# Kernel optimization log

Hardware: AMD Instinct MI355X
Metric: run time of the kernel (lower is better)

## Reference

```python
import jax, jax.numpy as jnp
from jax import lax
import numpy as np

NUM_TOKENS = 2048
HIDDEN = 768
MAX_SPAN_WIDTH = 20
NUM_CAND = NUM_TOKENS * MAX_SPAN_WIDTH  # 40960
FEAT = 20
UNARY = 1024
SPAN_DIM = 3 * HIDDEN + FEAT  # 2324
MAX_NUM_SPANS = 512
TOP_SPAN_RATIO = 0.4


def setup_inputs() -> dict:
    key = jax.random.key(0)
    ks = jax.random.split(key, 16)
    starts = jax.random.randint(ks[0], (NUM_CAND,), 0, NUM_TOKENS, dtype=jnp.int32)
    widths = jax.random.randint(ks[1], (NUM_CAND,), 0, MAX_SPAN_WIDTH, dtype=jnp.int32)
    ends = jnp.minimum(starts + widths, NUM_TOKENS - 1)
    p = lambda k, shp: (0.02 * jax.random.normal(k, shp, dtype=jnp.float32))
    return {
        "hidden_states": jax.random.normal(ks[2], (NUM_TOKENS, HIDDEN), dtype=jnp.float32),
        "candidate_starts": starts,
        "candidate_ends": ends,
        "speaker_ids": jax.random.randint(ks[3], (NUM_TOKENS,), 0, 2, dtype=jnp.int32),
        "w_attn": p(ks[4], (HIDDEN,)),
        "b_attn": p(ks[5], ()),
        "W1": p(ks[6], (SPAN_DIM, UNARY)),
        "b1": p(ks[7], (UNARY,)),
        "W2": p(ks[8], (UNARY,)),
        "b2": p(ks[9], ()),
        "emb_width": p(ks[10], (MAX_SPAN_WIDTH, FEAT)),
        "emb_width_prior": p(ks[11], (MAX_SPAN_WIDTH, FEAT)),
        "Wp1": p(ks[12], (FEAT, UNARY)),
        "bp1": p(ks[13], (UNARY,)),
        "Wp2": p(ks[14], (UNARY,)),
        "bp2": p(ks[15], ()),
    }


def extract_spans(starts, ends, scores, num_top, num_words):
    """Greedy NMS-style span pruning: take spans by descending score, rejecting
    spans that partially overlap (cross) an already-accepted span; return
    num_top accepted candidate indices sorted by (start, end)."""
    order = jnp.argsort(-scores)  # descending score
    s_sorted = starts[order]
    e_sorted = ends[order]
    tok = jnp.arange(num_words, dtype=jnp.int32)

    def step(carry, se):
        latest_end, earliest_start, count = carry
        s, e = se
        in_range = (tok >= s) & (tok <= e)
        cross = jnp.any(in_range & (tok > s) & (latest_end > e)) | \
                jnp.any(in_range & (tok < e) & (earliest_start < s))
        accept = jnp.logical_and(~cross, count < num_top)
        latest_end = jnp.where(accept, latest_end.at[s].max(e), latest_end)
        earliest_start = jnp.where(accept, earliest_start.at[e].min(s), earliest_start)
        count = count + accept.astype(jnp.int32)
        return (latest_end, earliest_start, count), accept

    init = (jnp.full((num_words,), -1, jnp.int32),
            jnp.full((num_words,), num_words, jnp.int32),
            jnp.int32(0))
    (_, _, count), accepted = lax.scan(step, init, (s_sorted, e_sorted))
    # sort accepted spans by (start, end); push rejected to the back
    BIG = jnp.int32(np.iinfo(np.int32).max)
    sort_key = jnp.where(accepted, s_sorted * (num_words + 1) + e_sorted, BIG)
    by_pos = jnp.argsort(sort_key)
    picked = order[by_pos[:num_top]]
    # pad (if fewer than num_top accepted) with the first accepted span
    valid = jnp.arange(num_top) < count
    return jnp.where(valid, picked, picked[0])


def reference(hidden_states, candidate_starts, candidate_ends, speaker_ids,
              w_attn, b_attn, W1, b1, W2, b2,
              emb_width, emb_width_prior, Wp1, bp1, Wp2, bp2):
    num_words = hidden_states.shape[0]
    num_top_spans = int(min(MAX_NUM_SPANS, num_words * TOP_SPAN_RATIO))

    # masked softmax attention pooling over each span's tokens
    tok_att = hidden_states @ w_attn + b_attn            # [T]
    doc = jnp.arange(num_words, dtype=jnp.int32)
    token_mask = (doc[None, :] >= candidate_starts[:, None]) & \
                 (doc[None, :] <= candidate_ends[:, None])  # [C, T]
    logits = jnp.where(token_mask, tok_att[None, :], -jnp.inf)
    token_attn = jax.nn.softmax(logits, axis=1)          # [C, T]
    attended = token_attn @ hidden_states                # [C, H]

    width_idx = candidate_ends - candidate_starts        # in [0, MAX_SPAN_WIDTH)
    span_emb = jnp.concatenate([
        hidden_states[candidate_starts],
        hidden_states[candidate_ends],
        emb_width[width_idx],
        attended,
    ], axis=1)                                           # [C, 3H+F]

    h = jax.nn.relu(span_emb @ W1 + b1)
    span_scores = h @ W2 + b2                            # [C]
    hp = jax.nn.relu(emb_width_prior[width_idx] @ Wp1 + bp1)
    span_scores = span_scores + (hp @ Wp2 + bp2)

    pruned_idx = extract_spans(candidate_starts, candidate_ends,
                               lax.stop_gradient(span_scores),
                               num_top_spans, num_words)
    pruned_starts = candidate_starts[pruned_idx]
    pruned_ends = candidate_ends[pruned_idx]
    pruned_emb = span_emb[pruned_idx]
    pruned_scores = span_scores[pruned_idx]
    pruned_speaker_ids = speaker_ids[pruned_starts]
    return (span_emb, pruned_idx, pruned_starts, pruned_ends,
            pruned_emb, pruned_scores, pruned_speaker_ids)
```

## Files before the change

### kernel.cpp

```cpp
#include <hip/hip_runtime.h>
#include <math.h>

#define NT 2048
#define HID 768
#define NC 40960
#define NFEAT 20
#define UN 1024
#define SDIM 2324
#define NTOP 512
#define WMAX 20
#define TOPT 8192

#define NCOLS 1793
#define CHUNK 64
#define NCHUNK 32
#define CS_STRIDE 1800

#define OFF_IDX   95191040
#define OFF_S     95191552
#define OFF_E     95192064
#define OFF_PEMB  95192576
#define OFF_SC    96382464
#define OFF_SP    96382976

__global__ void k_zero(int* __restrict__ p, int n) {
  int i = blockIdx.x * 256 + threadIdx.x;
  if (i < n) p[i] = 0;
}

__global__ void k_hist(const int* __restrict__ starts, int* __restrict__ hist) {
  int i = blockIdx.x * 256 + threadIdx.x;
  atomicAdd(&hist[starts[i]], 1);
}

__global__ __launch_bounds__(256) void k_prefix(const int* __restrict__ hist,
                                                int* __restrict__ cursor) {
  __shared__ int tsum[256];
  int tid = threadIdx.x;
  int v[8], pre[8];
  int s = 0;
  #pragma unroll
  for (int j = 0; j < 8; ++j) { v[j] = hist[tid * 8 + j]; pre[j] = s; s += v[j]; }
  tsum[tid] = s;
  __syncthreads();
  for (int off = 1; off < 256; off <<= 1) {
    int t = (tid >= off) ? tsum[tid - off] : 0;
    __syncthreads();
    tsum[tid] += t;
    __syncthreads();
  }
  int base = (tid > 0) ? tsum[tid - 1] : 0;
  #pragma unroll
  for (int j = 0; j < 8; ++j) cursor[tid * 8 + j] = base + pre[j];
}

__global__ void k_place(const int* __restrict__ starts, int* __restrict__ cursor,
                        int* __restrict__ ord) {
  int i = blockIdx.x * 256 + threadIdx.x;
  int pos = atomicAdd(&cursor[starts[i]], 1);
  ord[pos] = i;
}

__global__ __launch_bounds__(256) void k_tok_att(const float* __restrict__ hidden,
                                                 const float* __restrict__ w_attn,
                                                 const float* __restrict__ b_attn,
                                                 float* __restrict__ expA) {
  int wave = (blockIdx.x * blockDim.x + threadIdx.x) >> 6;
  int lane = threadIdx.x & 63;
  if (wave >= NT) return;
  const float* row = hidden + (size_t)wave * HID;
  float s = 0.f;
  for (int c = lane; c < HID; c += 64) s += row[c] * w_attn[c];
  #pragma unroll
  for (int off = 32; off; off >>= 1) s += __shfl_down(s, off);
  if (lane == 0) expA[wave] = expf(s + b_attn[0]);
}

__global__ __launch_bounds__(256) void k_pc(const float* __restrict__ emb_width,
                                            const float* __restrict__ W1,
                                            float* __restrict__ Pc) {
  int idx = blockIdx.x * 256 + threadIdx.x;
  int w = idx >> 10, j = idx & 1023;
  float s = 0.f;
  #pragma unroll
  for (int k = 0; k < NFEAT; ++k) s += emb_width[w * NFEAT + k] * W1[(size_t)(2 * HID + k) * UN + j];
  Pc[idx] = s;
}

__global__ __launch_bounds__(256) void k_prior(const float* __restrict__ ewp,
                                               const float* __restrict__ Wp1,
                                               const float* __restrict__ bp1,
                                               const float* __restrict__ Wp2,
                                               const float* __restrict__ bp2,
                                               float* __restrict__ prior) {
  int w = blockIdx.x;
  int tid = threadIdx.x;
  __shared__ float red[256];
  float local = 0.f;
  for (int j = tid; j < UN; j += 256) {
    float hp = bp1[j];
    #pragma unroll
    for (int k = 0; k < NFEAT; ++k) hp += ewp[w * NFEAT + k] * Wp1[k * UN + j];
    local += fmaxf(hp, 0.f) * Wp2[j];
  }
  red[tid] = local;
  __syncthreads();
  for (int st = 128; st > 0; st >>= 1) { if (tid < st) red[tid] += red[tid + st]; __syncthreads(); }
  if (tid == 0) prior[w] = red[0] + bp2[0];
}

__global__ __launch_bounds__(256) void k_matmul_P(const float* __restrict__ hidden,
                                                  const float* __restrict__ W1,
                                                  float* __restrict__ P) {
  __shared__ float As[16][132];
  __shared__ float Bs[16][128];
  int bn = blockIdx.x, bm = blockIdx.y;
  int n0 = bn * 128;
  int seg = n0 >> 10;
  int rowbase = (seg == 0) ? 0 : (seg == 1 ? HID : (2 * HID + NFEAT));
  int j0 = n0 & 1023;
  int tid = threadIdx.x;
  int tx = tid & 15, ty = tid >> 4;
  float acc[8][8] = {};
  for (int k0 = 0; k0 < HID; k0 += 16) {
    #pragma unroll
    for (int q = 0; q < 2; ++q) {
      int idx = q * 256 + tid;
      int m = idx >> 2, kg = idx & 3;
      float4 a = *(const float4*)&hidden[(size_t)(bm * 128 + m) * HID + k0 + kg * 4];
      As[kg * 4 + 0][m] = a.x; As[kg * 4 + 1][m] = a.y;
      As[kg * 4 + 2][m] = a.z; As[kg * 4 + 3][m] = a.w;
      int k = idx >> 5, ng = idx & 31;
      float4 b = *(const float4*)&W1[(size_t)(rowbase + k0 + k) * UN + j0 + ng * 4];
      *(float4*)&Bs[k][ng * 4] = b;
    }
    __syncthreads();
    #pragma unroll
    for (int k = 0; k < 16; ++k) {
      float4 a0 = *(const float4*)&As[k][ty * 8];
      float4 a1 = *(const float4*)&As[k][ty * 8 + 4];
      float4 b0 = *(const float4*)&Bs[k][tx * 8];
      float4 b1 = *(const float4*)&Bs[k][tx * 8 + 4];
      float av[8] = {a0.x, a0.y, a0.z, a0.w, a1.x, a1.y, a1.z, a1.w};
      float bv[8] = {b0.x, b0.y, b0.z, b0.w, b1.x, b1.y, b1.z, b1.w};
      #pragma unroll
      for (int i = 0; i < 8; ++i)
        #pragma unroll
        for (int jj = 0; jj < 8; ++jj) acc[i][jj] += av[i] * bv[jj];
    }
    __syncthreads();
  }
  #pragma unroll
  for (int i = 0; i < 8; ++i) {
    float* prow = &P[(size_t)(bm * 128 + ty * 8 + i) * 3072 + n0 + tx * 8];
    *(float4*)prow = make_float4(acc[i][0], acc[i][1], acc[i][2], acc[i][3]);
    *(float4*)(prow + 4) = make_float4(acc[i][4], acc[i][5], acc[i][6], acc[i][7]);
  }
}

__global__ __launch_bounds__(256) void k_psumA(const float* __restrict__ hidden,
                                               const float* __restrict__ P,
                                               const float* __restrict__ expA,
                                               double* __restrict__ chunkSum) {
  int col = blockIdx.x * 256 + threadIdx.x;
  int ch = blockIdx.y;
  if (col >= NCOLS) return;
  double acc = 0.0;
  int t0 = ch * CHUNK;
  if (col < HID) {
    const float* p = hidden + col;
    #pragma unroll 8
    for (int r = 0; r < CHUNK; ++r) {
      int t = t0 + r;
      acc += (double)expA[t] * (double)p[(size_t)t * HID];
    }
  } else if (col < HID + UN) {
    const float* p = P + 2048 + (col - HID);
    #pragma unroll 8
    for (int r = 0; r < CHUNK; ++r) {
      int t = t0 + r;
      acc += (double)expA[t] * (double)p[(size_t)t * 3072];
    }
  } else {
    #pragma unroll 8
    for (int r = 0; r < CHUNK; ++r) acc += (double)expA[t0 + r];
  }
  chunkSum[(size_t)ch * CS_STRIDE + col] = acc;
}

__global__ __launch_bounds__(256) void k_psumB(double* __restrict__ chunkSum,
                                               double* __restrict__ prefH,
                                               double* __restrict__ prefPd,
                                               double* __restrict__ prefZ) {
  int col = blockIdx.x * 256 + threadIdx.x;
  if (col >= NCOLS) return;
  double run = 0.0;
  for (int ch = 0; ch < NCHUNK; ++ch) {
    size_t o = (size_t)ch * CS_STRIDE + col;
    double v = chunkSum[o];
    chunkSum[o] = run;
    run += v;
  }
  if (col < HID) prefH[col] = 0.0;
  else if (col < HID + UN) prefPd[col - HID] = 0.0;
  else prefZ[0] = 0.0;
}

__global__ __launch_bounds__(256) void k_psumC(const float* __restrict__ hidden,
                                               const float* __restrict__ P,
                                               const float* __restrict__ expA,
                                               const double* __restrict__ chunkSum,
                                               double* __restrict__ prefH,
                                               double* __restrict__ prefPd,
                                               double* __restrict__ prefZ) {
  int col = blockIdx.x * 256 + threadIdx.x;
  int ch = blockIdx.y;
  if (col >= NCOLS) return;
  double acc = chunkSum[(size_t)ch * CS_STRIDE + col];
  int t0 = ch * CHUNK;
  if (col < HID) {
    const float* p = hidden + col;
    double* o = prefH + col;
    #pragma unroll 4
    for (int r = 0; r < CHUNK; ++r) {
      int t = t0 + r;
      acc += (double)expA[t] * (double)p[(size_t)t * HID];
      o[(size_t)(t + 1) * HID] = acc;
    }
  } else if (col < HID + UN) {
    int c = col - HID;
    const float* p = P + 2048 + c;
    double* o = prefPd + c;
    #pragma unroll 4
    for (int r = 0; r < CHUNK; ++r) {
      int t = t0 + r;
      acc += (double)expA[t] * (double)p[(size_t)t * 3072];
      o[(size_t)(t + 1) * UN] = acc;
    }
  } else {
    #pragma unroll 4
    for (int r = 0; r < CHUNK; ++r) {
      int t = t0 + r;
      acc += (double)expA[t];
      prefZ[t + 1] = acc;
    }
  }
}

__global__ __launch_bounds__(256) void k_span(
    const int* __restrict__ ord,
    const float* __restrict__ hidden, const int* __restrict__ starts, const int* __restrict__ ends,
    const float* __restrict__ emb_width,
    const double* __restrict__ prefH, const double* __restrict__ prefPd,
    const double* __restrict__ prefZ,
    const float* __restrict__ P, const float* __restrict__ Pc,
    const float* __restrict__ b1, const float* __restrict__ W2,
    const float* __restrict__ b2ptr, const float* __restrict__ prior,
    float* __restrict__ out, float* __restrict__ scores, unsigned long long* __restrict__ keys) {
  int i = ord[blockIdx.x];
  int s = starts[i], e = ends[i];
  int w = e - s;
  int tid = threadIdx.x;
  double invZ = 1.0 / (prefZ[e + 1] - prefZ[s]);
  const float* hs = hidden + (size_t)s * HID;
  const float* he = hidden + (size_t)e * HID;
  const double* pHs = prefH + (size_t)s * HID;
  const double* pHe = prefH + (size_t)(e + 1) * HID;
  float* orow = out + (size_t)i * SDIM;
  for (int q = tid; q < SDIM / 4; q += 256) {
    int c = q * 4;
    float4 v;
    if (c < HID) v = *(const float4*)(hs + c);
    else if (c < 2 * HID) v = *(const float4*)(he + (c - HID));
    else if (c < 2 * HID + NFEAT) v = *(const float4*)(emb_width + w * NFEAT + (c - 2 * HID));
    else {
      int cc = c - (2 * HID + NFEAT);
      const double* pe = pHe + cc;
      const double* ps = pHs + cc;
      v = make_float4((float)((pe[0] - ps[0]) * invZ),
                      (float)((pe[1] - ps[1]) * invZ),
                      (float)((pe[2] - ps[2]) * invZ),
                      (float)((pe[3] - ps[3]) * invZ));
    }
    *(float4*)(orow + c) = v;
  }
  int j = tid * 4;
  float4 pre = *(const float4*)(b1 + j);
  float4 pa = *(const float4*)(P + (size_t)s * 3072 + j);
  float4 pb = *(const float4*)(P + (size_t)e * 3072 + 1024 + j);
  float4 pc = *(const float4*)(Pc + w * UN + j);
  const double* pds = prefPd + (size_t)s * UN + j;
  const double* pde = prefPd + (size_t)(e + 1) * UN + j;
  pre.x += pa.x + pb.x + pc.x + (float)((pde[0] - pds[0]) * invZ);
  pre.y += pa.y + pb.y + pc.y + (float)((pde[1] - pds[1]) * invZ);
  pre.z += pa.z + pb.z + pc.z + (float)((pde[2] - pds[2]) * invZ);
  pre.w += pa.w + pb.w + pc.w + (float)((pde[3] - pds[3]) * invZ);
  float4 w2 = *(const float4*)(W2 + j);
  float local = fmaxf(pre.x, 0.f) * w2.x + fmaxf(pre.y, 0.f) * w2.y +
                fmaxf(pre.z, 0.f) * w2.z + fmaxf(pre.w, 0.f) * w2.w;
  #pragma unroll
  for (int off = 32; off; off >>= 1) local += __shfl_down(local, off);
  __shared__ float red[4];
  if ((tid & 63) == 0) red[tid >> 6] = local;
  __syncthreads();
  if (tid == 0) {
    float sc = red[0] + red[1] + red[2] + red[3] + b2ptr[0] + prior[w];
    scores[i] = sc;
    unsigned u = __float_as_uint(sc);
    u = (u >> 31) ? ~u : (u | 0x80000000u);
    unsigned inv = ~u;
    keys[i] = (((unsigned long long)inv) << 32) | (unsigned)i;
  }
}

__global__ void k_bucket(const unsigned long long* __restrict__ keys,
                         int* __restrict__ hist64k) {
  int i = blockIdx.x * 256 + threadIdx.x;
  atomicAdd(&hist64k[(int)(keys[i] >> 48)], 1);
}

__global__ __launch_bounds__(1024) void k_cutoff(const int* __restrict__ hist64k,
                                                 int* __restrict__ cutB) {
  __shared__ int psum[1024];
  int tid = threadIdx.x;
  int base = tid * 64;
  int s = 0;
  #pragma unroll
  for (int j = 0; j < 16; ++j) {
    int4 v = *(const int4*)&hist64k[base + j * 4];
    s += v.x + v.y + v.z + v.w;
  }
  psum[tid] = s;
  __syncthreads();
  for (int off = 1; off < 1024; off <<= 1) {
    int t = (tid >= off) ? psum[tid - off] : 0;
    __syncthreads();
    psum[tid] += t;
    __syncthreads();
  }
  int cumEnd = psum[tid];
  int cumStart = cumEnd - s;
  if (cumStart < TOPT && TOPT <= cumEnd) {
    int run = cumStart;
    for (int j = 0; j < 64; ++j) {
      run += hist64k[base + j];
      if (run >= TOPT) { cutB[0] = base + j; break; }
    }
  }
}

__global__ void k_compact(const unsigned long long* __restrict__ keys,
                          const int* __restrict__ cutB,
                          int* __restrict__ survCount,
                          int* __restrict__ surv,
                          unsigned long long* __restrict__ survKey) {
  int i = blockIdx.x * 256 + threadIdx.x;
  int B = cutB[0];
  unsigned long long k = keys[i];
  bool keep = ((int)(k >> 48)) <= B;
  unsigned long long m = __ballot(keep);
  if (m == 0ull) return;
  int lane = threadIdx.x & 63;
  int leader = __ffsll((long long)m) - 1;
  int pos = 0;
  if (lane == leader) pos = atomicAdd(survCount, __popcll(m));
  pos = __shfl(pos, leader);
  if (keep) {
    int slot = pos + __popcll(m & ((1ull << lane) - 1ull));
    surv[slot] = i;
    survKey[slot] = k;
  }
}

__global__ __launch_bounds__(256) void k_rankT(const unsigned long long* __restrict__ survKey,
                                               const int* __restrict__ survCount,
                                               int* __restrict__ rankS) {
  int S = survCount[0];
  int i = blockIdx.x * 256 + threadIdx.x;
  int j0 = blockIdx.y * 1280;
  if (i >= S || j0 >= S) return;
  int j1 = min(j0 + 1280, S);
  unsigned long long mk = survKey[i];
  int cnt = 0;
  for (int j = j0; j < j1; ++j) cnt += (survKey[j] < mk) ? 1 : 0;
  if (cnt) atomicAdd(&rankS[i], cnt);
}

__global__ void k_scatterT(const int* __restrict__ surv, const int* __restrict__ rankS,
                           const int* __restrict__ survCount, int* __restrict__ order) {
  int t = blockIdx.x * 256 + threadIdx.x;
  if (t < survCount[0]) order[rankS[t]] = surv[t];
}

__global__ void k_scanT(const int* __restrict__ order,
                        const int* __restrict__ starts,
                        const int* __restrict__ ends,
                        const int* __restrict__ survCount,
                        int* __restrict__ acc_idx, int* __restrict__ acc_s,
                        int* __restrict__ acc_e, int* __restrict__ acc_count,
                        int* __restrict__ flag) {
  __shared__ int LE[NT];
  __shared__ int ES[NT];
  int lane = threadIdx.x;
  int S = survCount[0];
  for (int t = lane; t < NT; t += 64) { LE[t] = -1; ES[t] = NT; }
  __syncthreads();
  int count = 0;
  for (int base = 0; base < S && count < NTOP; base += 64) {
    int idx = base + lane;
    bool valid = idx < S;
    int ci = order[valid ? idx : 0];
    int sv = starts[ci];
    int ev = ends[ci];
    bool pc = !valid;
    for (int t = sv; t <= ev; ++t) {
      int l = LE[t], es2 = ES[t];
      pc = pc || ((t > sv) && (l > ev)) || ((t < ev) && (es2 < sv));
    }
    unsigned long long rem = ~__ballot(pc);
    int localCount = 0;
    int ls = 0, le = -1, li = 0;
    while (rem != 0ull && count < NTOP) {
      int t = __ffsll((long long)rem) - 1;
      rem &= rem - 1;
      int s = __shfl(sv, t);
      int e = __shfl(ev, t);
      int cidx = __shfl(ci, t);
      bool ov = (lane < localCount) &&
                (((s < ls) && (ls <= e) && (e < le)) ||
                 ((ls < s) && (s <= le) && (le < e)));
      if (!__any(ov)) {
        if (lane == localCount) { ls = s; le = e; li = cidx; }
        localCount++;
        count++;
      }
    }
    int cbase = count - localCount;
    if (lane < localCount) {
      acc_idx[cbase + lane] = li;
      acc_s[cbase + lane] = ls;
      acc_e[cbase + lane] = le;
      atomicMax(&LE[ls], le);
      atomicMin(&ES[le], ls);
    }
    __syncthreads();
  }
  if (lane == 0) {
    acc_count[0] = count;
    flag[0] = (count < NTOP && S < NC) ? 1 : 0;
  }
}

__global__ __launch_bounds__(256) void k_rank_fb(const int* __restrict__ flag,
                                                 const unsigned long long* __restrict__ keys,
                                                 int* __restrict__ rank2) {
  if (!flag[0]) return;
  int ic = blockIdx.x >> 5;
  int jc = blockIdx.x & 31;
  int tid = threadIdx.x;
  int ibase = ic * 2048 + tid;
  unsigned long long mk[8];
  int cnt[8];
  #pragma unroll
  for (int k = 0; k < 8; ++k) { mk[k] = keys[ibase + k * 256]; cnt[k] = 0; }
  int j0 = jc * 1280;
  #pragma unroll 4
  for (int j = j0; j < j0 + 1280; ++j) {
    unsigned long long kj = keys[j];
    #pragma unroll
    for (int k = 0; k < 8; ++k) cnt[k] += (kj < mk[k]) ? 1 : 0;
  }
  #pragma unroll
  for (int k = 0; k < 8; ++k) if (cnt[k]) atomicAdd(&rank2[ibase + k * 256], cnt[k]);
}

__global__ void k_scatter_fb(const int* __restrict__ flag, const int* __restrict__ rank2,
                             int* __restrict__ orderFB) {
  if (!flag[0]) return;
  int i = blockIdx.x * 256 + threadIdx.x;
  orderFB[rank2[i]] = i;
}

__global__ void k_scan_fb(const int* __restrict__ flag,
                          const int* __restrict__ orderFB,
                          const int* __restrict__ starts,
                          const int* __restrict__ ends,
                          int* __restrict__ acc_idx, int* __restrict__ acc_s,
                          int* __restrict__ acc_e, int* __restrict__ acc_count) {
  if (!flag[0]) return;
  __shared__ int LE[NT];
  __shared__ int ES[NT];
  int lane = threadIdx.x;
  for (int t = lane; t < NT; t += 64) { LE[t] = -1; ES[t] = NT; }
  __syncthreads();
  int count = 0;
  for (int base = 0; base < NC && count < NTOP; base += 64) {
    int ci = orderFB[base + lane];
    int sv = starts[ci];
    int ev = ends[ci];
    bool pc = false;
    for (int t = sv; t <= ev; ++t) {
      int l = LE[t], es2 = ES[t];
      pc = pc || ((t > sv) && (l > ev)) || ((t < ev) && (es2 < sv));
    }
    unsigned long long rem = ~__ballot(pc);
    int localCount = 0;
    int ls = 0, le = -1, li = 0;
    while (rem != 0ull && count < NTOP) {
      int t = __ffsll((long long)rem) - 1;
      rem &= rem - 1;
      int s = __shfl(sv, t);
      int e = __shfl(ev, t);
      int cidx = __shfl(ci, t);
      bool ov = (lane < localCount) &&
                (((s < ls) && (ls <= e) && (e < le)) ||
                 ((ls < s) && (s <= le) && (le < e)));
      if (!__any(ov)) {
        if (lane == localCount) { ls = s; le = e; li = cidx; }
        localCount++;
        count++;
      }
    }
    int cbase = count - localCount;
    if (lane < localCount) {
      acc_idx[cbase + lane] = li;
      acc_s[cbase + lane] = ls;
      acc_e[cbase + lane] = le;
      atomicMax(&LE[ls], le);
      atomicMin(&ES[le], ls);
    }
    __syncthreads();
  }
  if (lane == 0) acc_count[0] = count;
}

__global__ __launch_bounds__(512) void k_outputs(const int* __restrict__ acc_idx,
                                                 const int* __restrict__ acc_s,
                                                 const int* __restrict__ acc_e,
                                                 const int* __restrict__ acc_count,
                                                 const float* __restrict__ scores,
                                                 const int* __restrict__ speaker,
                                                 float* __restrict__ out,
                                                 int* __restrict__ sortedIdx) {
  __shared__ int ks[NTOP];
  int tid = threadIdx.x;
  int count = acc_count[0];
  int key = 0x7FFFFFFF;
  if (tid < count) key = acc_s[tid] * (NT + 1) + acc_e[tid];
  ks[tid] = key;
  __syncthreads();
  if (tid < count) {
    int r = 0;
    for (int b = 0; b < count; ++b) {
      int kb = ks[b];
      r += ((kb < key) || (kb == key && b < tid)) ? 1 : 0;
    }
    int ci = acc_idx[tid];
    out[OFF_IDX + r] = (float)ci;
    out[OFF_S + r]   = (float)acc_s[tid];
    out[OFF_E + r]   = (float)acc_e[tid];
    out[OFF_SC + r]  = scores[ci];
    out[OFF_SP + r]  = (float)speaker[acc_s[tid]];
    sortedIdx[r] = ci;
  }
  __syncthreads();
  if (tid >= count) {
    out[OFF_IDX + tid] = out[OFF_IDX];
    out[OFF_S + tid]   = out[OFF_S];
    out[OFF_E + tid]   = out[OFF_E];
    out[OFF_SC + tid]  = out[OFF_SC];
    out[OFF_SP + tid]  = out[OFF_SP];
    sortedIdx[tid] = sortedIdx[0];
  }
}

__global__ __launch_bounds__(256) void k_copy_emb(const int* __restrict__ sortedIdx,
                                                  float* __restrict__ out) {
  int r = blockIdx.x;
  int ci = sortedIdx[r];
  const float* src = out + (size_t)ci * SDIM;
  float* dst = out + OFF_PEMB + (size_t)r * SDIM;
  for (int q = threadIdx.x; q < SDIM / 4; q += 256) {
    ((float4*)dst)[q] = ((const float4*)src)[q];
  }
}

extern "C" void kernel_launch(void* const* d_in, const int* in_sizes, int n_in,
                              void* d_out, int out_size, void* d_ws, size_t ws_size,
                              hipStream_t stream) {
  const float* hidden   = (const float*)d_in[0];
  const int*   starts   = (const int*)d_in[1];
  const int*   ends     = (const int*)d_in[2];
  const int*   speaker  = (const int*)d_in[3];
  const float* w_attn   = (const float*)d_in[4];
  const float* b_attn   = (const float*)d_in[5];
  const float* W1       = (const float*)d_in[6];
  const float* b1       = (const float*)d_in[7];
  const float* W2       = (const float*)d_in[8];
  const float* b2       = (const float*)d_in[9];
  const float* embw     = (const float*)d_in[10];
  const float* ewp      = (const float*)d_in[11];
  const float* Wp1      = (const float*)d_in[12];
  const float* bp1      = (const float*)d_in[13];
  const float* Wp2      = (const float*)d_in[14];
  const float* bp2      = (const float*)d_in[15];
  float* out = (float*)d_out;

  float* f = (float*)d_ws;
  float* P       = f;
  float* expA    = P + 6291456;
  float* Pc      = expA + 2048;
  float* prior   = Pc + 20480;
  float* scores  = prior + 32;
  unsigned long long* keys = (unsigned long long*)(scores + 40960);
  double* prefPd = (double*)(keys + 40960);
  double* prefZ  = prefPd + 2049 * 1024;
  double* chunkSum = prefZ + 2056;
  double* prefH  = chunkSum + 32 * CS_STRIDE;
  int* rankS     = (int*)(prefH + 2049 * 768);
  int* rank2     = rankS + 40960;
  int* order     = rank2 + 40960;
  int* orderFB   = order + 40960;
  int* acc_idx   = orderFB + 40960;
  int* acc_s     = acc_idx + NTOP;
  int* acc_e     = acc_s + NTOP;
  int* acc_count = acc_e + NTOP;
  int* flag      = acc_count + 4;
  int* sortedIdx = flag + 4;
  int* hist      = sortedIdx + NTOP;
  int* cursor    = hist + NT;
  int* ord       = cursor + NT;
  int* hist64k   = ord + 40960;
  int* survCount = hist64k + 65536;
  int* cutB      = survCount + 4;
  int* surv      = cutB + 4;
  unsigned long long* survKey = (unsigned long long*)(surv + 40960);

  k_zero<<<dim3(8), dim3(256), 0, stream>>>(hist, NT);
  k_zero<<<dim3(320), dim3(256), 0, stream>>>(rankS, 2 * NC);
  k_zero<<<dim3(257), dim3(256), 0, stream>>>(hist64k, 65536 + 8);

  k_hist<<<dim3(160), dim3(256), 0, stream>>>(starts, hist);
  k_prefix<<<dim3(1), dim3(256), 0, stream>>>(hist, cursor);
  k_place<<<dim3(160), dim3(256), 0, stream>>>(starts, cursor, ord);

  k_tok_att<<<dim3(512), dim3(256), 0, stream>>>(hidden, w_attn, b_attn, expA);
  k_pc<<<dim3(80), dim3(256), 0, stream>>>(embw, W1, Pc);
  k_prior<<<dim3(20), dim3(256), 0, stream>>>(ewp, Wp1, bp1, Wp2, bp2, prior);
  k_matmul_P<<<dim3(24, 16), dim3(256), 0, stream>>>(hidden, W1, P);

  k_psumA<<<dim3(8, NCHUNK), dim3(256), 0, stream>>>(hidden, P, expA, chunkSum);
  k_psumB<<<dim3(8), dim3(256), 0, stream>>>(chunkSum, prefH, prefPd, prefZ);
  k_psumC<<<dim3(8, NCHUNK), dim3(256), 0, stream>>>(hidden, P, expA, chunkSum,
                                                     prefH, prefPd, prefZ);

  k_span<<<dim3(NC), dim3(256), 0, stream>>>(ord, hidden, starts, ends, embw,
                                             prefH, prefPd, prefZ, P, Pc,
                                             b1, W2, b2, prior, out, scores, keys);

  k_bucket<<<dim3(160), dim3(256), 0, stream>>>(keys, hist64k);
  k_cutoff<<<dim3(1), dim3(1024), 0, stream>>>(hist64k, cutB);
  k_compact<<<dim3(160), dim3(256), 0, stream>>>(keys, cutB, survCount, surv, survKey);
  k_rankT<<<dim3(160, 32), dim3(256), 0, stream>>>(survKey, survCount, rankS);
  k_scatterT<<<dim3(160), dim3(256), 0, stream>>>(surv, rankS, survCount, order);
  k_scanT<<<dim3(1), dim3(64), 0, stream>>>(order, starts, ends, survCount,
                                            acc_idx, acc_s, acc_e, acc_count, flag);

  k_rank_fb<<<dim3(640), dim3(256), 0, stream>>>(flag, keys, rank2);
  k_scatter_fb<<<dim3(160), dim3(256), 0, stream>>>(flag, rank2, orderFB);
  k_scan_fb<<<dim3(1), dim3(64), 0, stream>>>(flag, orderFB, starts, ends,
                                              acc_idx, acc_s, acc_e, acc_count);

  k_outputs<<<dim3(1), dim3(512), 0, stream>>>(acc_idx, acc_s, acc_e, acc_count, scores,
                                               speaker, out, sortedIdx);
  k_copy_emb<<<dim3(NTOP), dim3(256), 0, stream>>>(sortedIdx, out);
}
```

Measured before the change: 1.002 ms.

## Fuse setup kernels, group span blocks by start token, fold bucket histogram

Merges the token-histogram, attention-logit, width-projection and prior kernels into one multi-role launch, and merges the three zeroing launches into one by reordering the workspace layout. The per-candidate span kernel becomes one block per start token that loops over that token's candidates, reusing the start-side loads of P, prefPd, prefZ and b1/W2 across the loop. The score-bucket histogram is now accumulated inside the span kernel, which removes the separate bucket pass. In exchange, only 2048 blocks of uneven size replace 40960 uniform ones, and each iteration of the serial per-block loop costs two barriers, which risks load imbalance and lower parallelism.

```diff
diff --git a/kernel.cpp b/kernel.cpp
--- a/kernel.cpp
+++ b/kernel.cpp
@@ -28,13 +28,66 @@
   if (i < n) p[i] = 0;
 }
 
-__global__ void k_hist(const int* __restrict__ starts, int* __restrict__ hist) {
-  int i = blockIdx.x * 256 + threadIdx.x;
-  atomicAdd(&hist[starts[i]], 1);
+__global__ __launch_bounds__(256) void k_setup(
+    const int* __restrict__ starts, int* __restrict__ hist,
+    const float* __restrict__ hidden, const float* __restrict__ w_attn,
+    const float* __restrict__ b_attn, float* __restrict__ expA,
+    const float* __restrict__ emb_width, const float* __restrict__ W1,
+    float* __restrict__ Pc,
+    const float* __restrict__ ewp, const float* __restrict__ Wp1,
+    const float* __restrict__ bp1, const float* __restrict__ Wp2,
+    const float* __restrict__ bp2, float* __restrict__ prior) {
+  __shared__ float red[256];
+  int b = blockIdx.x;
+  int tid = threadIdx.x;
+  if (b < 160) {
+    int i = b * 256 + tid;
+    atomicAdd(&hist[starts[i]], 1);
+    return;
+  }
+  b -= 160;
+  if (b < 512) {
+    int wave = (b * 256 + tid) >> 6;
+    int lane = tid & 63;
+    if (wave >= NT) return;
+    const float* row = hidden + (size_t)wave * HID;
+    float s = 0.f;
+    for (int c = lane; c < HID; c += 64) s += row[c] * w_attn[c];
+    #pragma unroll
+    for (int off = 32; off; off >>= 1) s += __shfl_down(s, off);
+    if (lane == 0) expA[wave] = expf(s + b_attn[0]);
+    return;
+  }
+  b -= 512;
+  if (b < 80) {
+    int idx = b * 256 + tid;
+    int w = idx >> 10, j = idx & 1023;
+    float s = 0.f;
+    #pragma unroll
+    for (int k = 0; k < NFEAT; ++k) s += emb_width[w * NFEAT + k] * W1[(size_t)(2 * HID + k) * UN + j];
+    Pc[idx] = s;
+    return;
+  }
+  b -= 80;
+  {
+    int w = b;
+    float local = 0.f;
+    for (int j = tid; j < UN; j += 256) {
+      float hp = bp1[j];
+      #pragma unroll
+      for (int k = 0; k < NFEAT; ++k) hp += ewp[w * NFEAT + k] * Wp1[k * UN + j];
+      local += fmaxf(hp, 0.f) * Wp2[j];
+    }
+    red[tid] = local;
+    __syncthreads();
+    for (int st = 128; st > 0; st >>= 1) { if (tid < st) red[tid] += red[tid + st]; __syncthreads(); }
+    if (tid == 0) prior[w] = red[0] + bp2[0];
+  }
 }
 
 __global__ __launch_bounds__(256) void k_prefix(const int* __restrict__ hist,
-                                                int* __restrict__ cursor) {
+                                                int* __restrict__ cursor,
+                                                int* __restrict__ bases) {
   __shared__ int tsum[256];
   int tid = threadIdx.x;
   int v[8], pre[8];
@@ -51,7 +104,11 @@
   }
   int base = (tid > 0) ? tsum[tid - 1] : 0;
   #pragma unroll
-  for (int j = 0; j < 8; ++j) cursor[tid * 8 + j] = base + pre[j];
+  for (int j = 0; j < 8; ++j) {
+    cursor[tid * 8 + j] = base + pre[j];
+    bases[tid * 8 + j] = base + pre[j];
+  }
+  if (tid == 255) bases[2048] = NC;
 }
 
 __global__ void k_place(const int* __restrict__ starts, int* __restrict__ cursor,
@@ -59,54 +116,6 @@
   int i = blockIdx.x * 256 + threadIdx.x;
   int pos = atomicAdd(&cursor[starts[i]], 1);
   ord[pos] = i;
-}
-
-__global__ __launch_bounds__(256) void k_tok_att(const float* __restrict__ hidden,
-                                                 const float* __restrict__ w_attn,
-                                                 const float* __restrict__ b_attn,
-                                                 float* __restrict__ expA) {
-  int wave = (blockIdx.x * blockDim.x + threadIdx.x) >> 6;
-  int lane = threadIdx.x & 63;
-  if (wave >= NT) return;
-  const float* row = hidden + (size_t)wave * HID;
-  float s = 0.f;
-  for (int c = lane; c < HID; c += 64) s += row[c] * w_attn[c];
-  #pragma unroll
-  for (int off = 32; off; off >>= 1) s += __shfl_down(s, off);
-  if (lane == 0) expA[wave] = expf(s + b_attn[0]);
-}
-
-__global__ __launch_bounds__(256) void k_pc(const float* __restrict__ emb_width,
-                                            const float* __restrict__ W1,
-                                            float* __restrict__ Pc) {
-  int idx = blockIdx.x * 256 + threadIdx.x;
-  int w = idx >> 10, j = idx & 1023;
-  float s = 0.f;
-  #pragma unroll
-  for (int k = 0; k < NFEAT; ++k) s += emb_width[w * NFEAT + k] * W1[(size_t)(2 * HID + k) * UN + j];
-  Pc[idx] = s;
-}
-
-__global__ __launch_bounds__(256) void k_prior(const float* __restrict__ ewp,
-                                               const float* __restrict__ Wp1,
-                                               const float* __restrict__ bp1,
-                                               const float* __restrict__ Wp2,
-                                               const float* __restrict__ bp2,
-                                               float* __restrict__ prior) {
-  int w = blockIdx.x;
-  int tid = threadIdx.x;
-  __shared__ float red[256];
-  float local = 0.f;
-  for (int j = tid; j < UN; j += 256) {
-    float hp = bp1[j];
-    #pragma unroll
-    for (int k = 0; k < NFEAT; ++k) hp += ewp[w * NFEAT + k] * Wp1[k * UN + j];
-    local += fmaxf(hp, 0.f) * Wp2[j];
-  }
-  red[tid] = local;
-  __syncthreads();
-  for (int st = 128; st > 0; st >>= 1) { if (tid < st) red[tid] += red[tid + st]; __syncthreads(); }
-  if (tid == 0) prior[w] = red[0] + bp2[0];
 }
 
 __global__ __launch_bounds__(256) void k_matmul_P(const float* __restrict__ hidden,
@@ -247,76 +256,83 @@
   }
 }
 
-__global__ __launch_bounds__(256) void k_span(
-    const int* __restrict__ ord,
-    const float* __restrict__ hidden, const int* __restrict__ starts, const int* __restrict__ ends,
+__global__ __launch_bounds__(256) void k_span2(
+    const int* __restrict__ ord, const int* __restrict__ bases,
+    const float* __restrict__ hidden, const int* __restrict__ ends,
     const float* __restrict__ emb_width,
     const double* __restrict__ prefH, const double* __restrict__ prefPd,
     const double* __restrict__ prefZ,
     const float* __restrict__ P, const float* __restrict__ Pc,
     const float* __restrict__ b1, const float* __restrict__ W2,
     const float* __restrict__ b2ptr, const float* __restrict__ prior,
-    float* __restrict__ out, float* __restrict__ scores, unsigned long long* __restrict__ keys) {
-  int i = ord[blockIdx.x];
-  int s = starts[i], e = ends[i];
-  int w = e - s;
+    float* __restrict__ out, float* __restrict__ scores,
+    unsigned long long* __restrict__ keys, int* __restrict__ hist64k) {
+  int s = blockIdx.x;
+  int c0 = bases[s], c1 = bases[s + 1];
+  if (c0 >= c1) return;
   int tid = threadIdx.x;
-  double invZ = 1.0 / (prefZ[e + 1] - prefZ[s]);
+  int j = tid * 4;
+  __shared__ float red[4];
+  float4 bb = *(const float4*)(b1 + j);
+  float4 pa = *(const float4*)(P + (size_t)s * 3072 + j);
+  float4 w2 = *(const float4*)(W2 + j);
+  const double* pdsp = prefPd + (size_t)s * UN + j;
+  double pds0 = pdsp[0], pds1 = pdsp[1], pds2 = pdsp[2], pds3 = pdsp[3];
+  double zs = prefZ[s];
   const float* hs = hidden + (size_t)s * HID;
-  const float* he = hidden + (size_t)e * HID;
   const double* pHs = prefH + (size_t)s * HID;
-  const double* pHe = prefH + (size_t)(e + 1) * HID;
-  float* orow = out + (size_t)i * SDIM;
-  for (int q = tid; q < SDIM / 4; q += 256) {
-    int c = q * 4;
-    float4 v;
-    if (c < HID) v = *(const float4*)(hs + c);
-    else if (c < 2 * HID) v = *(const float4*)(he + (c - HID));
-    else if (c < 2 * HID + NFEAT) v = *(const float4*)(emb_width + w * NFEAT + (c - 2 * HID));
-    else {
-      int cc = c - (2 * HID + NFEAT);
-      const double* pe = pHe + cc;
-      const double* ps = pHs + cc;
-      v = make_float4((float)((pe[0] - ps[0]) * invZ),
-                      (float)((pe[1] - ps[1]) * invZ),
-                      (float)((pe[2] - ps[2]) * invZ),
-                      (float)((pe[3] - ps[3]) * invZ));
-    }
-    *(float4*)(orow + c) = v;
-  }
-  int j = tid * 4;
-  float4 pre = *(const float4*)(b1 + j);
-  float4 pa = *(const float4*)(P + (size_t)s * 3072 + j);
-  float4 pb = *(const float4*)(P + (size_t)e * 3072 + 1024 + j);
-  float4 pc = *(const float4*)(Pc + w * UN + j);
-  const double* pds = prefPd + (size_t)s * UN + j;
-  const double* pde = prefPd + (size_t)(e + 1) * UN + j;
-  pre.x += pa.x + pb.x + pc.x + (float)((pde[0] - pds[0]) * invZ);
-  pre.y += pa.y + pb.y + pc.y + (float)((pde[1] - pds[1]) * invZ);
-  pre.z += pa.z + pb.z + pc.z + (float)((pde[2] - pds[2]) * invZ);
-  pre.w += pa.w + pb.w + pc.w + (float)((pde[3] - pds[3]) * invZ);
-  float4 w2 = *(const float4*)(W2 + j);
-  float local = fmaxf(pre.x, 0.f) * w2.x + fmaxf(pre.y, 0.f) * w2.y +
-                fmaxf(pre.z, 0.f) * w2.z + fmaxf(pre.w, 0.f) * w2.w;
-  #pragma unroll
-  for (int off = 32; off; off >>= 1) local += __shfl_down(local, off);
-  __shared__ float red[4];
-  if ((tid & 63) == 0) red[tid >> 6] = local;
-  __syncthreads();
-  if (tid == 0) {
-    float sc = red[0] + red[1] + red[2] + red[3] + b2ptr[0] + prior[w];
-    scores[i] = sc;
-    unsigned u = __float_as_uint(sc);
-    u = (u >> 31) ? ~u : (u | 0x80000000u);
-    unsigned inv = ~u;
-    keys[i] = (((unsigned long long)inv) << 32) | (unsigned)i;
-  }
-}
-
-__global__ void k_bucket(const unsigned long long* __restrict__ keys,
-                         int* __restrict__ hist64k) {
-  int i = blockIdx.x * 256 + threadIdx.x;
-  atomicAdd(&hist64k[(int)(keys[i] >> 48)], 1);
+  float b2v = b2ptr[0];
+
+  for (int c = c0; c < c1; ++c) {
+    int i = ord[c];
+    int e = ends[i];
+    int w = e - s;
+    double invZ = 1.0 / (prefZ[e + 1] - zs);
+    const float* he = hidden + (size_t)e * HID;
+    const double* pHe = prefH + (size_t)(e + 1) * HID;
+    float* orow = out + (size_t)i * SDIM;
+    for (int q = tid; q < SDIM / 4; q += 256) {
+      int cc = q * 4;
+      float4 v;
+      if (cc < HID) v = *(const float4*)(hs + cc);
+      else if (cc < 2 * HID) v = *(const float4*)(he + (cc - HID));
+      else if (cc < 2 * HID + NFEAT) v = *(const float4*)(emb_width + w * NFEAT + (cc - 2 * HID));
+      else {
+        int cx = cc - (2 * HID + NFEAT);
+        const double* pe = pHe + cx;
+        const double* ps = pHs + cx;
+        v = make_float4((float)((pe[0] - ps[0]) * invZ),
+                        (float)((pe[1] - ps[1]) * invZ),
+                        (float)((pe[2] - ps[2]) * invZ),
+                        (float)((pe[3] - ps[3]) * invZ));
+      }
+      *(float4*)(orow + cc) = v;
+    }
+    float4 pb = *(const float4*)(P + (size_t)e * 3072 + 1024 + j);
+    float4 pc = *(const float4*)(Pc + w * UN + j);
+    const double* pde = prefPd + (size_t)(e + 1) * UN + j;
+    float4 pre;
+    pre.x = bb.x + (pa.x + pb.x + pc.x + (float)((pde[0] - pds0) * invZ));
+    pre.y = bb.y + (pa.y + pb.y + pc.y + (float)((pde[1] - pds1) * invZ));
+    pre.z = bb.z + (pa.z + pb.z + pc.z + (float)((pde[2] - pds2) * invZ));
+    pre.w = bb.w + (pa.w + pb.w + pc.w + (float)((pde[3] - pds3) * invZ));
+    float local = fmaxf(pre.x, 0.f) * w2.x + fmaxf(pre.y, 0.f) * w2.y +
+                  fmaxf(pre.z, 0.f) * w2.z + fmaxf(pre.w, 0.f) * w2.w;
+    #pragma unroll
+    for (int off = 32; off; off >>= 1) local += __shfl_down(local, off);
+    if ((tid & 63) == 0) red[tid >> 6] = local;
+    __syncthreads();
+    if (tid == 0) {
+      float sc = red[0] + red[1] + red[2] + red[3] + b2v + prior[w];
+      scores[i] = sc;
+      unsigned u = __float_as_uint(sc);
+      u = (u >> 31) ? ~u : (u | 0x80000000u);
+      unsigned inv = ~u;
+      keys[i] = (((unsigned long long)inv) << 32) | (unsigned)i;
+      atomicAdd(&hist64k[(int)(inv >> 16)], 1);
+    }
+    __syncthreads();
+  }
 }
 
 __global__ __launch_bounds__(1024) void k_cutoff(const int* __restrict__ hist64k,
@@ -619,7 +635,11 @@
   double* prefH  = chunkSum + 32 * CS_STRIDE;
   int* rankS     = (int*)(prefH + 2049 * 768);
   int* rank2     = rankS + 40960;
-  int* order     = rank2 + 40960;
+  int* hist      = rank2 + 40960;
+  int* hist64k   = hist + 2048;
+  int* survCount = hist64k + 65536;
+  int* cutB      = survCount + 4;
+  int* order     = cutB + 4;
   int* orderFB   = order + 40960;
   int* acc_idx   = orderFB + 40960;
   int* acc_s     = acc_idx + NTOP;
@@ -627,26 +647,19 @@
   int* acc_count = acc_e + NTOP;
   int* flag      = acc_count + 4;
   int* sortedIdx = flag + 4;
-  int* hist      = sortedIdx + NTOP;
-  int* cursor    = hist + NT;
-  int* ord       = cursor + NT;
-  int* hist64k   = ord + 40960;
-  int* survCount = hist64k + 65536;
-  int* cutB      = survCount + 4;
-  int* surv      = cutB + 4;
+  int* cursor    = sortedIdx + NTOP;
+  int* bases     = cursor + NT;
+  int* ord       = bases + 2056;
+  int* surv      = ord + 40960;
   unsigned long long* survKey = (unsigned long long*)(surv + 40960);
 
-  k_zero<<<dim3(8), dim3(256), 0, stream>>>(hist, NT);
-  k_zero<<<dim3(320), dim3(256), 0, stream>>>(rankS, 2 * NC);
-  k_zero<<<dim3(257), dim3(256), 0, stream>>>(hist64k, 65536 + 8);
-
-  k_hist<<<dim3(160), dim3(256), 0, stream>>>(starts, hist);
-  k_prefix<<<dim3(1), dim3(256), 0, stream>>>(hist, cursor);
+  k_zero<<<dim3(585), dim3(256), 0, stream>>>(rankS, 149512);
+
+  k_setup<<<dim3(772), dim3(256), 0, stream>>>(starts, hist, hidden, w_attn, b_attn, expA,
+                                               embw, W1, Pc, ewp, Wp1, bp1, Wp2, bp2, prior);
+  k_prefix<<<dim3(1), dim3(256), 0, stream>>>(hist, cursor, bases);
   k_place<<<dim3(160), dim3(256), 0, stream>>>(starts, cursor, ord);
 
-  k_tok_att<<<dim3(512), dim3(256), 0, stream>>>(hidden, w_attn, b_attn, expA);
-  k_pc<<<dim3(80), dim3(256), 0, stream>>>(embw, W1, Pc);
-  k_prior<<<dim3(20), dim3(256), 0, stream>>>(ewp, Wp1, bp1, Wp2, bp2, prior);
   k_matmul_P<<<dim3(24, 16), dim3(256), 0, stream>>>(hidden, W1, P);
 
   k_psumA<<<dim3(8, NCHUNK), dim3(256), 0, stream>>>(hidden, P, expA, chunkSum);
@@ -654,11 +667,10 @@
   k_psumC<<<dim3(8, NCHUNK), dim3(256), 0, stream>>>(hidden, P, expA, chunkSum,
                                                      prefH, prefPd, prefZ);
 
-  k_span<<<dim3(NC), dim3(256), 0, stream>>>(ord, hidden, starts, ends, embw,
-                                             prefH, prefPd, prefZ, P, Pc,
-                                             b1, W2, b2, prior, out, scores, keys);
-
-  k_bucket<<<dim3(160), dim3(256), 0, stream>>>(keys, hist64k);
+  k_span2<<<dim3(NT), dim3(256), 0, stream>>>(ord, bases, hidden, ends, embw,
+                                              prefH, prefPd, prefZ, P, Pc,
+                                              b1, W2, b2, prior, out, scores, keys, hist64k);
+
   k_cutoff<<<dim3(1), dim3(1024), 0, stream>>>(hist64k, cutB);
   k_compact<<<dim3(160), dim3(256), 0, stream>>>(keys, cutB, survCount, surv, survKey);
   k_rankT<<<dim3(160, 32), dim3(256), 0, stream>>>(survKey, survCount, rankS);
```

After: 1.026 ms. 1.02x slower.

## Fuse independent prologue kernels and merge histogram, output and copy launches

Applied to the files above, without the earlier changes.

Several small independent kernels (matmul P, start histogram, token attention, Pc, prior) become one launch that dispatches work by block index. The 64k bucket histogram moves into k_span, and the three zeroing launches become one after the workspace buffers are reordered to be contiguous. k_outputs and k_copy_emb are merged into a per-row kernel that computes each rank with a block reduction. The aim is to cut launch overhead and serialization, at the cost of a heavier mixed-role kernel and an atomic inside k_span.

```diff
diff --git a/kernel.cpp b/kernel.cpp
--- a/kernel.cpp
+++ b/kernel.cpp
@@ -28,9 +28,110 @@
   if (i < n) p[i] = 0;
 }
 
-__global__ void k_hist(const int* __restrict__ starts, int* __restrict__ hist) {
-  int i = blockIdx.x * 256 + threadIdx.x;
-  atomicAdd(&hist[starts[i]], 1);
+__global__ __launch_bounds__(256) void k_fused0(
+    const float* __restrict__ hidden, const float* __restrict__ W1,
+    float* __restrict__ P,
+    const int* __restrict__ starts, int* __restrict__ hist,
+    const float* __restrict__ w_attn, const float* __restrict__ b_attn,
+    float* __restrict__ expA,
+    const float* __restrict__ emb_width, float* __restrict__ Pc,
+    const float* __restrict__ ewp, const float* __restrict__ Wp1,
+    const float* __restrict__ bp1, const float* __restrict__ Wp2,
+    const float* __restrict__ bp2, float* __restrict__ prior) {
+  __shared__ float smem[16 * 132 + 16 * 128];
+  int b = blockIdx.x;
+  int tid = threadIdx.x;
+  if (b < 384) {
+    float (*As)[132] = (float(*)[132])smem;
+    float (*Bs)[128] = (float(*)[128])(smem + 16 * 132);
+    int bn = b % 24, bm = b / 24;
+    int n0 = bn * 128;
+    int seg = n0 >> 10;
+    int rowbase = (seg == 0) ? 0 : (seg == 1 ? HID : (2 * HID + NFEAT));
+    int j0 = n0 & 1023;
+    int tx = tid & 15, ty = tid >> 4;
+    float acc[8][8] = {};
+    for (int k0 = 0; k0 < HID; k0 += 16) {
+      #pragma unroll
+      for (int q = 0; q < 2; ++q) {
+        int idx = q * 256 + tid;
+        int m = idx >> 2, kg = idx & 3;
+        float4 a = *(const float4*)&hidden[(size_t)(bm * 128 + m) * HID + k0 + kg * 4];
+        As[kg * 4 + 0][m] = a.x; As[kg * 4 + 1][m] = a.y;
+        As[kg * 4 + 2][m] = a.z; As[kg * 4 + 3][m] = a.w;
+        int k = idx >> 5, ng = idx & 31;
+        float4 bv4 = *(const float4*)&W1[(size_t)(rowbase + k0 + k) * UN + j0 + ng * 4];
+        *(float4*)&Bs[k][ng * 4] = bv4;
+      }
+      __syncthreads();
+      #pragma unroll
+      for (int k = 0; k < 16; ++k) {
+        float4 a0 = *(const float4*)&As[k][ty * 8];
+        float4 a1 = *(const float4*)&As[k][ty * 8 + 4];
+        float4 b0 = *(const float4*)&Bs[k][tx * 8];
+        float4 b1 = *(const float4*)&Bs[k][tx * 8 + 4];
+        float av[8] = {a0.x, a0.y, a0.z, a0.w, a1.x, a1.y, a1.z, a1.w};
+        float bv[8] = {b0.x, b0.y, b0.z, b0.w, b1.x, b1.y, b1.z, b1.w};
+        #pragma unroll
+        for (int i = 0; i < 8; ++i)
+          #pragma unroll
+          for (int jj = 0; jj < 8; ++jj) acc[i][jj] += av[i] * bv[jj];
+      }
+      __syncthreads();
+    }
+    #pragma unroll
+    for (int i = 0; i < 8; ++i) {
+      float* prow = &P[(size_t)(bm * 128 + ty * 8 + i) * 3072 + n0 + tx * 8];
+      *(float4*)prow = make_float4(acc[i][0], acc[i][1], acc[i][2], acc[i][3]);
+      *(float4*)(prow + 4) = make_float4(acc[i][4], acc[i][5], acc[i][6], acc[i][7]);
+    }
+    return;
+  }
+  b -= 384;
+  if (b < 160) {
+    int i = b * 256 + tid;
+    atomicAdd(&hist[starts[i]], 1);
+    return;
+  }
+  b -= 160;
+  if (b < 512) {
+    int wave = (b * 256 + tid) >> 6;
+    int lane = tid & 63;
+    if (wave >= NT) return;
+    const float* row = hidden + (size_t)wave * HID;
+    float s = 0.f;
+    for (int c = lane; c < HID; c += 64) s += row[c] * w_attn[c];
+    #pragma unroll
+    for (int off = 32; off; off >>= 1) s += __shfl_down(s, off);
+    if (lane == 0) expA[wave] = expf(s + b_attn[0]);
+    return;
+  }
+  b -= 512;
+  if (b < 80) {
+    int idx = b * 256 + tid;
+    int w = idx >> 10, j = idx & 1023;
+    float s = 0.f;
+    #pragma unroll
+    for (int k = 0; k < NFEAT; ++k) s += emb_width[w * NFEAT + k] * W1[(size_t)(2 * HID + k) * UN + j];
+    Pc[idx] = s;
+    return;
+  }
+  b -= 80;
+  {
+    float* red = smem;
+    int w = b;
+    float local = 0.f;
+    for (int j = tid; j < UN; j += 256) {
+      float hp = bp1[j];
+      #pragma unroll
+      for (int k = 0; k < NFEAT; ++k) hp += ewp[w * NFEAT + k] * Wp1[k * UN + j];
+      local += fmaxf(hp, 0.f) * Wp2[j];
+    }
+    red[tid] = local;
+    __syncthreads();
+    for (int st = 128; st > 0; st >>= 1) { if (tid < st) red[tid] += red[tid + st]; __syncthreads(); }
+    if (tid == 0) prior[w] = red[0] + bp2[0];
+  }
 }
 
 __global__ __launch_bounds__(256) void k_prefix(const int* __restrict__ hist,
@@ -59,103 +160,6 @@
   int i = blockIdx.x * 256 + threadIdx.x;
   int pos = atomicAdd(&cursor[starts[i]], 1);
   ord[pos] = i;
-}
-
-__global__ __launch_bounds__(256) void k_tok_att(const float* __restrict__ hidden,
-                                                 const float* __restrict__ w_attn,
-                                                 const float* __restrict__ b_attn,
-                                                 float* __restrict__ expA) {
-  int wave = (blockIdx.x * blockDim.x + threadIdx.x) >> 6;
-  int lane = threadIdx.x & 63;
-  if (wave >= NT) return;
-  const float* row = hidden + (size_t)wave * HID;
-  float s = 0.f;
-  for (int c = lane; c < HID; c += 64) s += row[c] * w_attn[c];
-  #pragma unroll
-  for (int off = 32; off; off >>= 1) s += __shfl_down(s, off);
-  if (lane == 0) expA[wave] = expf(s + b_attn[0]);
-}
-
-__global__ __launch_bounds__(256) void k_pc(const float* __restrict__ emb_width,
-                                            const float* __restrict__ W1,
-                                            float* __restrict__ Pc) {
-  int idx = blockIdx.x * 256 + threadIdx.x;
-  int w = idx >> 10, j = idx & 1023;
-  float s = 0.f;
-  #pragma unroll
-  for (int k = 0; k < NFEAT; ++k) s += emb_width[w * NFEAT + k] * W1[(size_t)(2 * HID + k) * UN + j];
-  Pc[idx] = s;
-}
-
-__global__ __launch_bounds__(256) void k_prior(const float* __restrict__ ewp,
-                                               const float* __restrict__ Wp1,
-                                               const float* __restrict__ bp1,
-                                               const float* __restrict__ Wp2,
-                                               const float* __restrict__ bp2,
-                                               float* __restrict__ prior) {
-  int w = blockIdx.x;
-  int tid = threadIdx.x;
-  __shared__ float red[256];
-  float local = 0.f;
-  for (int j = tid; j < UN; j += 256) {
-    float hp = bp1[j];
-    #pragma unroll
-    for (int k = 0; k < NFEAT; ++k) hp += ewp[w * NFEAT + k] * Wp1[k * UN + j];
-    local += fmaxf(hp, 0.f) * Wp2[j];
-  }
-  red[tid] = local;
-  __syncthreads();
-  for (int st = 128; st > 0; st >>= 1) { if (tid < st) red[tid] += red[tid + st]; __syncthreads(); }
-  if (tid == 0) prior[w] = red[0] + bp2[0];
-}
-
-__global__ __launch_bounds__(256) void k_matmul_P(const float* __restrict__ hidden,
-                                                  const float* __restrict__ W1,
-                                                  float* __restrict__ P) {
-  __shared__ float As[16][132];
-  __shared__ float Bs[16][128];
-  int bn = blockIdx.x, bm = blockIdx.y;
-  int n0 = bn * 128;
-  int seg = n0 >> 10;
-  int rowbase = (seg == 0) ? 0 : (seg == 1 ? HID : (2 * HID + NFEAT));
-  int j0 = n0 & 1023;
-  int tid = threadIdx.x;
-  int tx = tid & 15, ty = tid >> 4;
-  float acc[8][8] = {};
-  for (int k0 = 0; k0 < HID; k0 += 16) {
-    #pragma unroll
-    for (int q = 0; q < 2; ++q) {
-      int idx = q * 256 + tid;
-      int m = idx >> 2, kg = idx & 3;
-      float4 a = *(const float4*)&hidden[(size_t)(bm * 128 + m) * HID + k0 + kg * 4];
-      As[kg * 4 + 0][m] = a.x; As[kg * 4 + 1][m] = a.y;
-      As[kg * 4 + 2][m] = a.z; As[kg * 4 + 3][m] = a.w;
-      int k = idx >> 5, ng = idx & 31;
-      float4 b = *(const float4*)&W1[(size_t)(rowbase + k0 + k) * UN + j0 + ng * 4];
-      *(float4*)&Bs[k][ng * 4] = b;
-    }
-    __syncthreads();
-    #pragma unroll
-    for (int k = 0; k < 16; ++k) {
-      float4 a0 = *(const float4*)&As[k][ty * 8];
-      float4 a1 = *(const float4*)&As[k][ty * 8 + 4];
-      float4 b0 = *(const float4*)&Bs[k][tx * 8];
-      float4 b1 = *(const float4*)&Bs[k][tx * 8 + 4];
-      float av[8] = {a0.x, a0.y, a0.z, a0.w, a1.x, a1.y, a1.z, a1.w};
-      float bv[8] = {b0.x, b0.y, b0.z, b0.w, b1.x, b1.y, b1.z, b1.w};
-      #pragma unroll
-      for (int i = 0; i < 8; ++i)
-        #pragma unroll
-        for (int jj = 0; jj < 8; ++jj) acc[i][jj] += av[i] * bv[jj];
-    }
-    __syncthreads();
-  }
-  #pragma unroll
-  for (int i = 0; i < 8; ++i) {
-    float* prow = &P[(size_t)(bm * 128 + ty * 8 + i) * 3072 + n0 + tx * 8];
-    *(float4*)prow = make_float4(acc[i][0], acc[i][1], acc[i][2], acc[i][3]);
-    *(float4*)(prow + 4) = make_float4(acc[i][4], acc[i][5], acc[i][6], acc[i][7]);
-  }
 }
 
 __global__ __launch_bounds__(256) void k_psumA(const float* __restrict__ hidden,
@@ -256,7 +260,8 @@
     const float* __restrict__ P, const float* __restrict__ Pc,
     const float* __restrict__ b1, const float* __restrict__ W2,
     const float* __restrict__ b2ptr, const float* __restrict__ prior,
-    float* __restrict__ out, float* __restrict__ scores, unsigned long long* __restrict__ keys) {
+    float* __restrict__ out, float* __restrict__ scores,
+    unsigned long long* __restrict__ keys, int* __restrict__ hist64k) {
   int i = ord[blockIdx.x];
   int s = starts[i], e = ends[i];
   int w = e - s;
@@ -310,13 +315,8 @@
     u = (u >> 31) ? ~u : (u | 0x80000000u);
     unsigned inv = ~u;
     keys[i] = (((unsigned long long)inv) << 32) | (unsigned)i;
-  }
-}
-
-__global__ void k_bucket(const unsigned long long* __restrict__ keys,
-                         int* __restrict__ hist64k) {
-  int i = blockIdx.x * 256 + threadIdx.x;
-  atomicAdd(&hist64k[(int)(keys[i] >> 48)], 1);
+    atomicAdd(&hist64k[(int)(inv >> 16)], 1);
+  }
 }
 
 __global__ __launch_bounds__(1024) void k_cutoff(const int* __restrict__ hist64k,
@@ -534,53 +534,59 @@
   if (lane == 0) acc_count[0] = count;
 }
 
-__global__ __launch_bounds__(512) void k_outputs(const int* __restrict__ acc_idx,
-                                                 const int* __restrict__ acc_s,
-                                                 const int* __restrict__ acc_e,
-                                                 const int* __restrict__ acc_count,
-                                                 const float* __restrict__ scores,
-                                                 const int* __restrict__ speaker,
-                                                 float* __restrict__ out,
-                                                 int* __restrict__ sortedIdx) {
+__global__ __launch_bounds__(256) void k_out_copy(
+    const int* __restrict__ acc_idx, const int* __restrict__ acc_s,
+    const int* __restrict__ acc_e, const int* __restrict__ acc_count,
+    const float* __restrict__ scores, const int* __restrict__ speaker,
+    float* __restrict__ out) {
   __shared__ int ks[NTOP];
+  __shared__ int redi[256];
+  __shared__ long long redl[256];
+  int b = blockIdx.x;
   int tid = threadIdx.x;
   int count = acc_count[0];
-  int key = 0x7FFFFFFF;
-  if (tid < count) key = acc_s[tid] * (NT + 1) + acc_e[tid];
-  ks[tid] = key;
+  for (int q = tid; q < NTOP; q += 256)
+    ks[q] = (q < count) ? acc_s[q] * (NT + 1) + acc_e[q] : 0x7FFFFFFF;
   __syncthreads();
-  if (tid < count) {
-    int r = 0;
-    for (int b = 0; b < count; ++b) {
-      int kb = ks[b];
-      r += ((kb < key) || (kb == key && b < tid)) ? 1 : 0;
-    }
-    int ci = acc_idx[tid];
+  int r, ci, sv, ev;
+  if (b < count) {
+    int key = ks[b];
+    int cnt = 0;
+    for (int q = tid; q < count; q += 256) {
+      int kb = ks[q];
+      cnt += ((kb < key) || (kb == key && q < b)) ? 1 : 0;
+    }
+    redi[tid] = cnt;
+    __syncthreads();
+    for (int st = 128; st > 0; st >>= 1) { if (tid < st) redi[tid] += redi[tid + st]; __syncthreads(); }
+    r = redi[0];
+    ci = acc_idx[b]; sv = acc_s[b]; ev = acc_e[b];
+  } else {
+    long long best = 0x7FFFFFFFFFFFLL;
+    for (int q = tid; q < count; q += 256) {
+      long long p = ((long long)ks[q] << 10) | q;
+      best = (p < best) ? p : best;
+    }
+    redl[tid] = best;
+    __syncthreads();
+    for (int st = 128; st > 0; st >>= 1) {
+      if (tid < st) redl[tid] = (redl[tid + st] < redl[tid]) ? redl[tid + st] : redl[tid];
+      __syncthreads();
+    }
+    int j0 = (int)(redl[0] & 1023);
+    r = b;
+    ci = acc_idx[j0]; sv = acc_s[j0]; ev = acc_e[j0];
+  }
+  if (tid == 0) {
     out[OFF_IDX + r] = (float)ci;
-    out[OFF_S + r]   = (float)acc_s[tid];
-    out[OFF_E + r]   = (float)acc_e[tid];
+    out[OFF_S + r]   = (float)sv;
+    out[OFF_E + r]   = (float)ev;
     out[OFF_SC + r]  = scores[ci];
-    out[OFF_SP + r]  = (float)speaker[acc_s[tid]];
-    sortedIdx[r] = ci;
-  }
-  __syncthreads();
-  if (tid >= count) {
-    out[OFF_IDX + tid] = out[OFF_IDX];
-    out[OFF_S + tid]   = out[OFF_S];
-    out[OFF_E + tid]   = out[OFF_E];
-    out[OFF_SC + tid]  = out[OFF_SC];
-    out[OFF_SP + tid]  = out[OFF_SP];
-    sortedIdx[tid] = sortedIdx[0];
-  }
-}
-
-__global__ __launch_bounds__(256) void k_copy_emb(const int* __restrict__ sortedIdx,
-                                                  float* __restrict__ out) {
-  int r = blockIdx.x;
-  int ci = sortedIdx[r];
+    out[OFF_SP + r]  = (float)speaker[sv];
+  }
   const float* src = out + (size_t)ci * SDIM;
   float* dst = out + OFF_PEMB + (size_t)r * SDIM;
-  for (int q = threadIdx.x; q < SDIM / 4; q += 256) {
+  for (int q = tid; q < SDIM / 4; q += 256) {
     ((float4*)dst)[q] = ((const float4*)src)[q];
   }
 }
@@ -619,35 +625,29 @@
   double* prefH  = chunkSum + 32 * CS_STRIDE;
   int* rankS     = (int*)(prefH + 2049 * 768);
   int* rank2     = rankS + 40960;
-  int* order     = rank2 + 40960;
+  int* hist      = rank2 + 40960;
+  int* hist64k   = hist + 2048;
+  int* survCount = hist64k + 65536;
+  int* cutB      = survCount + 4;
+  int* order     = cutB + 4;
   int* orderFB   = order + 40960;
   int* acc_idx   = orderFB + 40960;
   int* acc_s     = acc_idx + NTOP;
   int* acc_e     = acc_s + NTOP;
   int* acc_count = acc_e + NTOP;
   int* flag      = acc_count + 4;
-  int* sortedIdx = flag + 4;
-  int* hist      = sortedIdx + NTOP;
-  int* cursor    = hist + NT;
+  int* cursor    = flag + 4;
   int* ord       = cursor + NT;
-  int* hist64k   = ord + 40960;
-  int* survCount = hist64k + 65536;
-  int* cutB      = survCount + 4;
-  int* surv      = cutB + 4;
+  int* surv      = ord + 40960;
   unsigned long long* survKey = (unsigned long long*)(surv + 40960);
 
-  k_zero<<<dim3(8), dim3(256), 0, stream>>>(hist, NT);
-  k_zero<<<dim3(320), dim3(256), 0, stream>>>(rankS, 2 * NC);
-  k_zero<<<dim3(257), dim3(256), 0, stream>>>(hist64k, 65536 + 8);
-
-  k_hist<<<dim3(160), dim3(256), 0, stream>>>(starts, hist);
+  k_zero<<<dim3(585), dim3(256), 0, stream>>>(rankS, 149512);
+
+  k_fused0<<<dim3(1156), dim3(256), 0, stream>>>(hidden, W1, P, starts, hist,
+                                                 w_attn, b_attn, expA, embw, Pc,
+                                                 ewp, Wp1, bp1, Wp2, bp2, prior);
   k_prefix<<<dim3(1), dim3(256), 0, stream>>>(hist, cursor);
   k_place<<<dim3(160), dim3(256), 0, stream>>>(starts, cursor, ord);
-
-  k_tok_att<<<dim3(512), dim3(256), 0, stream>>>(hidden, w_attn, b_attn, expA);
-  k_pc<<<dim3(80), dim3(256), 0, stream>>>(embw, W1, Pc);
-  k_prior<<<dim3(20), dim3(256), 0, stream>>>(ewp, Wp1, bp1, Wp2, bp2, prior);
-  k_matmul_P<<<dim3(24, 16), dim3(256), 0, stream>>>(hidden, W1, P);
 
   k_psumA<<<dim3(8, NCHUNK), dim3(256), 0, stream>>>(hidden, P, expA, chunkSum);
   k_psumB<<<dim3(8), dim3(256), 0, stream>>>(chunkSum, prefH, prefPd, prefZ);
@@ -656,9 +656,8 @@
 
   k_span<<<dim3(NC), dim3(256), 0, stream>>>(ord, hidden, starts, ends, embw,
                                              prefH, prefPd, prefZ, P, Pc,
-                                             b1, W2, b2, prior, out, scores, keys);
-
-  k_bucket<<<dim3(160), dim3(256), 0, stream>>>(keys, hist64k);
+                                             b1, W2, b2, prior, out, scores, keys, hist64k);
+
   k_cutoff<<<dim3(1), dim3(1024), 0, stream>>>(hist64k, cutB);
   k_compact<<<dim3(160), dim3(256), 0, stream>>>(keys, cutB, survCount, surv, survKey);
   k_rankT<<<dim3(160, 32), dim3(256), 0, stream>>>(survKey, survCount, rankS);
@@ -671,7 +670,6 @@
   k_scan_fb<<<dim3(1), dim3(64), 0, stream>>>(flag, orderFB, starts, ends,
                                               acc_idx, acc_s, acc_e, acc_count);
 
-  k_outputs<<<dim3(1), dim3(512), 0, stream>>>(acc_idx, acc_s, acc_e, acc_count, scores,
-                                               speaker, out, sortedIdx);
-  k_copy_emb<<<dim3(NTOP), dim3(256), 0, stream>>>(sortedIdx, out);
-}
+  k_out_copy<<<dim3(NTOP), dim3(256), 0, stream>>>(acc_idx, acc_s, acc_e, acc_count,
+                                                   scores, speaker, out);
+}
```

New measurement: 945.6 us. 5.6% less time.
